# Optimization experiments

Hardware: AMD Instinct MI355X
Metric: run time of the kernel (lower is better)

## Reference

```python
import jax, jax.numpy as jnp
import numpy as np
import math

B, S, D = 2, 2048, 1024
H = 16
DK = D // H  # dim_k == dim_v == 64


def setup_inputs() -> dict:
    key = jax.random.key(0)
    ks = jax.random.split(key, 8)
    scale = 1.0 / math.sqrt(D)
    inp = {
        "query": jax.random.normal(ks[0], (B, S, D), dtype=jnp.float32),
        "key": jax.random.normal(ks[1], (B, S, D), dtype=jnp.float32),
        "value": jax.random.normal(ks[2], (B, S, D), dtype=jnp.float32),
        # stacked per-head projection weights (torch Linear y = x @ W.T; here stored as [H, D, DK])
        "Wq": jax.random.uniform(ks[3], (H, D, DK), dtype=jnp.float32, minval=-scale, maxval=scale),
        "Wk": jax.random.uniform(ks[4], (H, D, DK), dtype=jnp.float32, minval=-scale, maxval=scale),
        "Wv": jax.random.uniform(ks[5], (H, D, DK), dtype=jnp.float32, minval=-scale, maxval=scale),
        "Wo": jax.random.uniform(ks[6], (D, H * DK), dtype=jnp.float32, minval=-scale, maxval=scale),
        "bo": jax.random.uniform(ks[7], (D,), dtype=jnp.float32, minval=-scale, maxval=scale),
    }
    return inp


def reference(query, key, value, Wq, Wk, Wv, Wo, bo):
    # per-head projections, batched over heads via einsum
    q = jnp.einsum("bsd,hdk->bhsk", query, Wq)   # [B,H,S,DK]
    k = jnp.einsum("btd,hdk->bhtk", key, Wk)     # [B,H,S,DK]
    v = jnp.einsum("btd,hdv->bhtv", value, Wv)   # [B,H,S,DK]
    scores = jnp.einsum("bhsk,bhtk->bhst", q, k) / jnp.sqrt(jnp.float32(DK))
    # causal mask (is_causal=True): strictly upper triangle -> -inf
    causal = jnp.tril(jnp.ones((S, S), dtype=bool))  # True = keep
    scores = jnp.where(causal[None, None], scores, -jnp.inf)
    attn = jax.nn.softmax(scores, axis=-1)
    # NaN correction (no-op under pure causal masking, kept for faithfulness)
    attn = jnp.where(jnp.isnan(attn), 0.0, attn)
    out = jnp.einsum("bhst,bhtv->bhsv", attn, v)  # [B,H,S,DK]
    out = jnp.transpose(out, (0, 2, 1, 3)).reshape(B, S, H * DK)  # concat heads
    return out @ Wo.T + bo
```

## Files before the change

### kernel.cpp

```cpp
#include <hip/hip_runtime.h>


#define B_ 2
#define S_ 2048
#define D_ 1024
#define H_ 16
#define DK_ 64
#define NEG_BIG (-1e30f)

typedef unsigned short u16;
typedef __attribute__((ext_vector_type(8))) short bf16x8;
typedef __attribute__((ext_vector_type(4))) float f32x4;

__device__ __forceinline__ float b2f(u16 v) {
    union { unsigned u; float f; } x; x.u = ((unsigned)v) << 16; return x.f;
}
__device__ __forceinline__ u16 f2b(float f) {
    union { float f; unsigned u; } x; x.f = f;
    unsigned r = x.u + 0x7fff + ((x.u >> 16) & 1);
    return (u16)(r >> 16);
}
__device__ __forceinline__ u16 f2b_fast(float f) {
    union { float f; unsigned u; } x; x.f = f;
    return (u16)((x.u + 0x8000u) >> 16);
}

__device__ __forceinline__ bool is_f32(const void* p) {
    const unsigned* u = (const unsigned*)p;
    int cnt = 0;
#pragma unroll
    for (int i = 0; i < 64; i++) {
        unsigned e = (u[i * 8] >> 7) & 0xFFu;
        cnt += (e >= 110u && e <= 134u) ? 1 : 0;
    }
    return cnt < 32;
}

template<bool F32>
__device__ __forceinline__ bf16x8 load8(const void* p, size_t idx) {
    if constexpr (F32) {
        const float* f = (const float*)p + idx;
        float4 a = *(const float4*)f;
        float4 b = *(const float4*)(f + 4);
        bf16x8 r;
        ((u16*)&r)[0] = f2b(a.x); ((u16*)&r)[1] = f2b(a.y);
        ((u16*)&r)[2] = f2b(a.z); ((u16*)&r)[3] = f2b(a.w);
        ((u16*)&r)[4] = f2b(b.x); ((u16*)&r)[5] = f2b(b.y);
        ((u16*)&r)[6] = f2b(b.z); ((u16*)&r)[7] = f2b(b.w);
        return r;
    } else {
        return *(const bf16x8*)((const u16*)p + idx);
    }
}

__global__ __launch_bounds__(256) void wtrans(const void* Wq, const void* Wk, const void* Wv,
                                              u16* WqT, u16* WkT, u16* WvT) {
    __shared__ __align__(16) u16 Ts[64][72];
    const int t = threadIdx.x;
    const int k0 = blockIdx.x * 64;
    const int h = blockIdx.y;
    const int wsel = blockIdx.z;
    const void* W = (wsel == 0) ? Wq : (wsel == 1) ? Wk : Wv;
    u16* WT = (wsel == 0) ? WqT : (wsel == 1) ? WkT : WvT;
    const bool wf = is_f32(W);

    const int drow = t >> 2, c0 = (t & 3) * 16;
    size_t sidx = ((size_t)h * D_ + k0 + drow) * DK_ + c0;
    bf16x8 v0, v1;
    if (wf) { v0 = load8<true >(W, sidx); v1 = load8<true >(W, sidx + 8); }
    else    { v0 = load8<false>(W, sidx); v1 = load8<false>(W, sidx + 8); }
    *(bf16x8*)&Ts[drow][c0]     = v0;
    *(bf16x8*)&Ts[drow][c0 + 8] = v1;
    __syncthreads();

    const int nrow = t >> 2, kc0 = (t & 3) * 16;
    u16 tmp[16];
#pragma unroll
    for (int j = 0; j < 16; j++) tmp[j] = Ts[kc0 + j][nrow];
    u16* dst = &WT[((size_t)h * DK_ + nrow) * D_ + k0 + kc0];
    *(bf16x8*)&dst[0] = *(const bf16x8*)&tmp[0];
    *(bf16x8*)&dst[8] = *(const bf16x8*)&tmp[8];
}

template<bool AF32>
__device__ void qproj_body(const void* A, const u16* WT, u16* Qt, int bb,
                           u16 (*As)[64][72], u16 (*Wt)[64][72]) {
    const int tid = threadIdx.x, mt = blockIdx.x, h = blockIdx.y;
    const int w = tid >> 6, lane = tid & 63, quad = lane >> 4, ln = lane & 15;
    const int s0 = mt * 64;
    const int row = tid >> 3, col = (tid & 7) * 8;
    const int row1 = row + 32;
    const int brow = tid >> 2, bc0 = (tid & 3) * 16;
    const size_t wbase = ((size_t)h * DK_ + brow) * D_ + bc0;

    bf16x8 areg0, areg1, breg0, breg1;
    areg0 = load8<AF32>(A, ((size_t)bb * S_ + s0 + row ) * D_ + col);
    areg1 = load8<AF32>(A, ((size_t)bb * S_ + s0 + row1) * D_ + col);
    breg0 = *(const bf16x8*)&WT[wbase];
    breg1 = *(const bf16x8*)&WT[wbase + 8];

    f32x4 acc[4];
#pragma unroll
    for (int t = 0; t < 4; t++)
#pragma unroll
        for (int r = 0; r < 4; r++) acc[t][r] = 0.f;

    int buf = 0;
    for (int k0 = 0; k0 < D_; k0 += 64, buf ^= 1) {
        *(bf16x8*)&As[buf][row ][col] = areg0;
        *(bf16x8*)&As[buf][row1][col] = areg1;
        *(bf16x8*)&Wt[buf][brow][bc0    ] = breg0;
        *(bf16x8*)&Wt[buf][brow][bc0 + 8] = breg1;
        __syncthreads();
        if (k0 + 64 < D_) {
            areg0 = load8<AF32>(A, ((size_t)bb * S_ + s0 + row ) * D_ + k0 + 64 + col);
            areg1 = load8<AF32>(A, ((size_t)bb * S_ + s0 + row1) * D_ + k0 + 64 + col);
            breg0 = *(const bf16x8*)&WT[wbase + k0 + 64];
            breg1 = *(const bf16x8*)&WT[wbase + k0 + 64 + 8];
        }
#pragma unroll
        for (int kk = 0; kk < 2; kk++) {
            bf16x8 a = *(const bf16x8*)&As[buf][w * 16 + ln][kk * 32 + quad * 8];
#pragma unroll
            for (int t = 0; t < 4; t++) {
                bf16x8 bm = *(const bf16x8*)&Wt[buf][t * 16 + ln][kk * 32 + quad * 8];
                acc[t] = __builtin_amdgcn_mfma_f32_16x16x32_bf16(a, bm, acc[t], 0, 0, 0);
            }
        }
    }

#pragma unroll
    for (int t = 0; t < 4; t++)
#pragma unroll
        for (int r = 0; r < 4; r++)
            Qt[((size_t)bb * S_ + s0 + w * 16 + quad * 4 + r) * D_ + h * DK_ + t * 16 + ln] =
                f2b(acc[t][r] * 0.125f);
}

__global__ __launch_bounds__(256) void qproj(const void* query, const u16* WqT, u16* Qt) {
    __shared__ __align__(16) u16 As[2][64][72];
    __shared__ __align__(16) u16 Wt[2][64][72];
    const int bb = blockIdx.z;
    if (is_f32(query)) qproj_body<true >(query, WqT, Qt, bb, As, Wt);
    else               qproj_body<false>(query, WqT, Qt, bb, As, Wt);
}

template<bool AF32>
__device__ void projkv_body(const void* A, const u16* WT, u16* Ko, u16* VTo,
                            int bb, int which, u16 (*As)[64][72], u16 (*Wt)[64][72]) {
    const int tid = threadIdx.x, mt = blockIdx.x, h = blockIdx.y;
    const int w = tid >> 6, lane = tid & 63, quad = lane >> 4, ln = lane & 15;
    const int s0 = mt * 64;
    const int row = tid >> 3, col = (tid & 7) * 8;
    const int row1 = row + 32;
    const int brow = tid >> 2, bc0 = (tid & 3) * 16;
    const size_t wbase = ((size_t)h * DK_ + brow) * D_ + bc0;

    bf16x8 areg0, areg1, breg0, breg1;
    areg0 = load8<AF32>(A, ((size_t)bb * S_ + s0 + row ) * D_ + col);
    areg1 = load8<AF32>(A, ((size_t)bb * S_ + s0 + row1) * D_ + col);
    breg0 = *(const bf16x8*)&WT[wbase];
    breg1 = *(const bf16x8*)&WT[wbase + 8];

    f32x4 acc[4];
#pragma unroll
    for (int t = 0; t < 4; t++)
#pragma unroll
        for (int r = 0; r < 4; r++) acc[t][r] = 0.f;

    int buf = 0;
    for (int k0 = 0; k0 < D_; k0 += 64, buf ^= 1) {
        *(bf16x8*)&As[buf][row ][col] = areg0;
        *(bf16x8*)&As[buf][row1][col] = areg1;
        *(bf16x8*)&Wt[buf][brow][bc0    ] = breg0;
        *(bf16x8*)&Wt[buf][brow][bc0 + 8] = breg1;
        __syncthreads();
        if (k0 + 64 < D_) {
            areg0 = load8<AF32>(A, ((size_t)bb * S_ + s0 + row ) * D_ + k0 + 64 + col);
            areg1 = load8<AF32>(A, ((size_t)bb * S_ + s0 + row1) * D_ + k0 + 64 + col);
            breg0 = *(const bf16x8*)&WT[wbase + k0 + 64];
            breg1 = *(const bf16x8*)&WT[wbase + k0 + 64 + 8];
        }
#pragma unroll
        for (int kk = 0; kk < 2; kk++) {
            bf16x8 a = *(const bf16x8*)&As[buf][w * 16 + ln][kk * 32 + quad * 8];
#pragma unroll
            for (int t = 0; t < 4; t++) {
                bf16x8 bm = *(const bf16x8*)&Wt[buf][t * 16 + ln][kk * 32 + quad * 8];
                acc[t] = __builtin_amdgcn_mfma_f32_16x16x32_bf16(a, bm, acc[t], 0, 0, 0);
            }
        }
    }

    if (which == 0) {
#pragma unroll
        for (int t = 0; t < 4; t++)
#pragma unroll
            for (int r = 0; r < 4; r++)
                Ko[((size_t)h * S_ + s0 + w * 16 + quad * 4 + r) * DK_ + t * 16 + ln] =
                    f2b(acc[t][r]);
    } else {
#pragma unroll
        for (int t = 0; t < 4; t++)
#pragma unroll
            for (int r = 0; r < 4; r++)
                Wt[0][t * 16 + ln][w * 16 + quad * 4 + r] = f2b(acc[t][r]);
        __syncthreads();
        *(bf16x8*)&VTo[((size_t)h * DK_ + row ) * S_ + s0 + col] = *(const bf16x8*)&Wt[0][row ][col];
        *(bf16x8*)&VTo[((size_t)h * DK_ + row1) * S_ + s0 + col] = *(const bf16x8*)&Wt[0][row1][col];
    }
}

__global__ __launch_bounds__(256) void projkv(const void* key, const void* value,
                                              const u16* WkT, const u16* WvT,
                                              u16* KVbase, int bb) {
    __shared__ __align__(16) u16 As[2][64][72];
    __shared__ __align__(16) u16 Wt[2][64][72];
    const int which = blockIdx.z;
    const void* A = which ? value : key;
    const u16* WT = which ? WvT : WkT;
    u16* Ko  = KVbase;
    u16* VTo = KVbase + (size_t)H_ * S_ * DK_;
    if (is_f32(A)) projkv_body<true >(A, WT, Ko, VTo, bb, which, As, Wt);
    else           projkv_body<false>(A, WT, Ko, VTo, bb, which, As, Wt);
}

__global__ __launch_bounds__(256) void flashq(u16* __restrict__ Xq,
                                              const u16* __restrict__ KV,
                                              int bb0, size_t zstride) {
    __shared__ __align__(16) u16 BufA[2][64][72];
    __shared__ __align__(16) u16 BufB[2][64][72];
    __shared__ __align__(16) u16 Ps[4][32][72];
    const int tid = threadIdx.x;
    const int bx = (int)blockIdx.x;
    const int qt = (blockIdx.z & 1) ? bx : ((int)gridDim.x - 1 - bx);
    const int h = blockIdx.y;
    const int bb = bb0 + blockIdx.z;
    const u16* Kb  = KV + (size_t)blockIdx.z * zstride;
    const u16* VTb = Kb + (size_t)H_ * S_ * DK_;
    const int w = tid >> 6, lane = tid & 63, quad = lane >> 4, ln = lane & 15;
    const int s0 = qt * 128;
    const int row = tid >> 3, col = (tid & 7) * 8;
    const int row1 = row + 32;
    const int j0max = 2 * qt;
    const int jmax  = 2 * qt + 1;

    bf16x8 kreg0 = *(const bf16x8*)&Kb [((size_t)h * S_  + row ) * DK_ + col];
    bf16x8 kreg1 = *(const bf16x8*)&Kb [((size_t)h * S_  + row1) * DK_ + col];
    bf16x8 vreg0 = *(const bf16x8*)&VTb[((size_t)h * DK_ + row ) * S_  + col];
    bf16x8 vreg1 = *(const bf16x8*)&VTb[((size_t)h * DK_ + row1) * S_  + col];

    *(bf16x8*)&BufA[0][row ][col] = *(const bf16x8*)&Xq[((size_t)bb * S_ + s0 + row ) * D_ + h * DK_ + col];
    *(bf16x8*)&BufA[0][row1][col] = *(const bf16x8*)&Xq[((size_t)bb * S_ + s0 + row1) * D_ + h * DK_ + col];
    *(bf16x8*)&BufA[1][row ][col] = *(const bf16x8*)&Xq[((size_t)bb * S_ + s0 + 64 + row ) * D_ + h * DK_ + col];
    *(bf16x8*)&BufA[1][row1][col] = *(const bf16x8*)&Xq[((size_t)bb * S_ + s0 + 64 + row1) * D_ + h * DK_ + col];
    __syncthreads();
    bf16x8 qa0_0 = *(const bf16x8*)&BufA[0][w * 16 + ln][quad * 8];
    bf16x8 qa1_0 = *(const bf16x8*)&BufA[0][w * 16 + ln][32 + quad * 8];
    bf16x8 qa0_1 = *(const bf16x8*)&BufA[1][w * 16 + ln][quad * 8];
    bf16x8 qa1_1 = *(const bf16x8*)&BufA[1][w * 16 + ln][32 + quad * 8];
    __syncthreads();

    f32x4 O0[4], O1[4];
    float psum0[4], psum1[4];
#pragma unroll
    for (int t = 0; t < 4; t++)
#pragma unroll
        for (int r = 0; r < 4; r++) { O0[t][r] = 0.f; O1[t][r] = 0.f; }
#pragma unroll
    for (int r = 0; r < 4; r++) { psum0[r] = 0.f; psum1[r] = 0.f; }

    for (int j = 0; j <= jmax; j++) {
        const int buf = j & 1;
        *(bf16x8*)&BufA[buf][row ][col] = kreg0;
        *(bf16x8*)&BufA[buf][row1][col] = kreg1;
        *(bf16x8*)&BufB[buf][row ][col] = vreg0;
        *(bf16x8*)&BufB[buf][row1][col] = vreg1;
        __syncthreads();

        if (j < jmax) {
            kreg0 = *(const bf16x8*)&Kb [((size_t)h * S_  + (j + 1) * 64 + row ) * DK_ + col];
            kreg1 = *(const bf16x8*)&Kb [((size_t)h * S_  + (j + 1) * 64 + row1) * DK_ + col];
            vreg0 = *(const bf16x8*)&VTb[((size_t)h * DK_ + row ) * S_ + (j + 1) * 64 + col];
            vreg1 = *(const bf16x8*)&VTb[((size_t)h * DK_ + row1) * S_ + (j + 1) * 64 + col];
        }

        const bool act0 = (j <= j0max);

        if (act0) {
            f32x4 sf[4];
#pragma unroll
            for (int t = 0; t < 4; t++)
#pragma unroll
                for (int r = 0; r < 4; r++) sf[t][r] = 0.f;
#pragma unroll
            for (int kk = 0; kk < 2; kk++) {
                bf16x8 a = kk ? qa1_0 : qa0_0;
#pragma unroll
                for (int t = 0; t < 4; t++) {
                    bf16x8 bm = *(const bf16x8*)&BufA[buf][t * 16 + ln][kk * 32 + quad * 8];
                    sf[t] = __builtin_amdgcn_mfma_f32_16x16x32_bf16(a, bm, sf[t], 0, 0, 0);
                }
            }
            if (j == j0max) {
#pragma unroll
                for (int t = 0; t < 4; t++) {
                    int keyl = t * 16 + ln;
#pragma unroll
                    for (int r = 0; r < 4; r++) {
                        int qr = w * 16 + quad * 4 + r;
                        if (keyl > qr) sf[t][r] = NEG_BIG;
                    }
                }
            }
#pragma unroll
            for (int t = 0; t < 4; t++)
#pragma unroll
                for (int r = 0; r < 4; r++) {
                    float p = __expf(sf[t][r]);
                    psum0[r] += p;
                    Ps[w][quad * 4 + r][t * 16 + ln] = f2b_fast(p);
                }
        }

        {
            f32x4 sf[4];
#pragma unroll
            for (int t = 0; t < 4; t++)
#pragma unroll
                for (int r = 0; r < 4; r++) sf[t][r] = 0.f;
#pragma unroll
            for (int kk = 0; kk < 2; kk++) {
                bf16x8 a = kk ? qa1_1 : qa0_1;
#pragma unroll
                for (int t = 0; t < 4; t++) {
                    bf16x8 bm = *(const bf16x8*)&BufA[buf][t * 16 + ln][kk * 32 + quad * 8];
                    sf[t] = __builtin_amdgcn_mfma_f32_16x16x32_bf16(a, bm, sf[t], 0, 0, 0);
                }
            }
            if (j == jmax) {
#pragma unroll
                for (int t = 0; t < 4; t++) {
                    int keyl = t * 16 + ln;
#pragma unroll
                    for (int r = 0; r < 4; r++) {
                        int qr = w * 16 + quad * 4 + r;
                        if (keyl > qr) sf[t][r] = NEG_BIG;
                    }
                }
            }
#pragma unroll
            for (int t = 0; t < 4; t++)
#pragma unroll
                for (int r = 0; r < 4; r++) {
                    float p = __expf(sf[t][r]);
                    psum1[r] += p;
                    Ps[w][16 + quad * 4 + r][t * 16 + ln] = f2b_fast(p);
                }
        }
        __syncthreads();

        if (act0) {
#pragma unroll
            for (int kk = 0; kk < 2; kk++) {
                bf16x8 a = *(const bf16x8*)&Ps[w][ln][kk * 32 + quad * 8];
#pragma unroll
                for (int t = 0; t < 4; t++) {
                    bf16x8 bm = *(const bf16x8*)&BufB[buf][t * 16 + ln][kk * 32 + quad * 8];
                    O0[t] = __builtin_amdgcn_mfma_f32_16x16x32_bf16(a, bm, O0[t], 0, 0, 0);
                }
            }
        }
#pragma unroll
        for (int kk = 0; kk < 2; kk++) {
            bf16x8 a = *(const bf16x8*)&Ps[w][16 + ln][kk * 32 + quad * 8];
#pragma unroll
            for (int t = 0; t < 4; t++) {
                bf16x8 bm = *(const bf16x8*)&BufB[buf][t * 16 + ln][kk * 32 + quad * 8];
                O1[t] = __builtin_amdgcn_mfma_f32_16x16x32_bf16(a, bm, O1[t], 0, 0, 0);
            }
        }
    }

#pragma unroll
    for (int r = 0; r < 4; r++) {
        float s = psum0[r];
        s += __shfl_xor(s, 1, 64);
        s += __shfl_xor(s, 2, 64);
        s += __shfl_xor(s, 4, 64);
        s += __shfl_xor(s, 8, 64);
        float inv = 1.0f / s;
        int sr = s0 + w * 16 + quad * 4 + r;
#pragma unroll
        for (int t = 0; t < 4; t++) {
            Xq[((size_t)bb * S_ + sr) * D_ + h * DK_ + t * 16 + ln] = f2b(O0[t][r] * inv);
        }
    }
#pragma unroll
    for (int r = 0; r < 4; r++) {
        float s = psum1[r];
        s += __shfl_xor(s, 1, 64);
        s += __shfl_xor(s, 2, 64);
        s += __shfl_xor(s, 4, 64);
        s += __shfl_xor(s, 8, 64);
        float inv = 1.0f / s;
        int sr = s0 + 64 + w * 16 + quad * 4 + r;
#pragma unroll
        for (int t = 0; t < 4; t++) {
            Xq[((size_t)bb * S_ + sr) * D_ + h * DK_ + t * 16 + ln] = f2b(O1[t][r] * inv);
        }
    }
}

__global__ __launch_bounds__(256) void copyx(const u16* __restrict__ src,
                                             u16* __restrict__ dst) {
    size_t i = ((size_t)blockIdx.x * 256 + threadIdx.x) * 8;
    *(bf16x8*)&dst[i] = *(const bf16x8*)&src[i];
}

template<bool WF32>
__device__ void outgemm_body(const u16* X, const void* Wo, const void* bo, bool bf32,
                             float* Y, u16 (*As)[64][72], u16 (*Bs)[64][72]) {
    const int tid = threadIdx.x, mt = blockIdx.x, nt = blockIdx.y;
    const int w = tid >> 6, lane = tid & 63, quad = lane >> 4, ln = lane & 15;
    const int m0 = mt * 64, n0 = nt * 64;
    const int row = tid >> 3, col = (tid & 7) * 8;
    const int row1 = row + 32;

    bf16x8 areg0, areg1, wreg0, wreg1;
    areg0 = *(const bf16x8*)&X[(size_t)(m0 + row ) * D_ + col];
    areg1 = *(const bf16x8*)&X[(size_t)(m0 + row1) * D_ + col];
    wreg0 = load8<WF32>(Wo, (size_t)(n0 + row ) * D_ + col);
    wreg1 = load8<WF32>(Wo, (size_t)(n0 + row1) * D_ + col);

    f32x4 acc[4];
#pragma unroll
    for (int t = 0; t < 4; t++)
#pragma unroll
        for (int r = 0; r < 4; r++) acc[t][r] = 0.f;

    int buf = 0;
    for (int k0 = 0; k0 < D_; k0 += 64, buf ^= 1) {
        *(bf16x8*)&As[buf][row ][col] = areg0;
        *(bf16x8*)&As[buf][row1][col] = areg1;
        *(bf16x8*)&Bs[buf][row ][col] = wreg0;
        *(bf16x8*)&Bs[buf][row1][col] = wreg1;
        __syncthreads();
        if (k0 + 64 < D_) {
            areg0 = *(const bf16x8*)&X[(size_t)(m0 + row ) * D_ + k0 + 64 + col];
            areg1 = *(const bf16x8*)&X[(size_t)(m0 + row1) * D_ + k0 + 64 + col];
            wreg0 = load8<WF32>(Wo, (size_t)(n0 + row ) * D_ + k0 + 64 + col);
            wreg1 = load8<WF32>(Wo, (size_t)(n0 + row1) * D_ + k0 + 64 + col);
        }
#pragma unroll
        for (int kk = 0; kk < 2; kk++) {
            bf16x8 a = *(const bf16x8*)&As[buf][w * 16 + ln][kk * 32 + quad * 8];
#pragma unroll
            for (int t = 0; t < 4; t++) {
                bf16x8 bm = *(const bf16x8*)&Bs[buf][t * 16 + ln][kk * 32 + quad * 8];
                acc[t] = __builtin_amdgcn_mfma_f32_16x16x32_bf16(a, bm, acc[t], 0, 0, 0);
            }
        }
    }

#pragma unroll
    for (int t = 0; t < 4; t++) {
        int n = n0 + t * 16 + ln;
        float bias = bf32 ? ((const float*)bo)[n] : b2f(((const u16*)bo)[n]);
#pragma unroll
        for (int r = 0; r < 4; r++) {
            int m = m0 + w * 16 + quad * 4 + r;
            Y[(size_t)m * D_ + n] = acc[t][r] + bias;
        }
    }
}

__global__ __launch_bounds__(256) void outgemm(const u16* __restrict__ X,
                                               const void* Wo, const void* bo,
                                               float* __restrict__ Y) {
    __shared__ __align__(16) u16 As[2][64][72];
    __shared__ __align__(16) u16 Bs[2][64][72];
    const bool wf = is_f32(Wo), bf = is_f32(bo);
    if (wf) outgemm_body<true >(X, Wo, bo, bf, Y, As, Bs);
    else    outgemm_body<false>(X, Wo, bo, bf, Y, As, Bs);
}

extern "C" void kernel_launch(void* const* d_in, const int* in_sizes, int n_in,
                              void* d_out, int out_size, void* d_ws, size_t ws_size,
                              hipStream_t stream) {
    const void* q  = d_in[0];
    const void* k  = d_in[1];
    const void* v  = d_in[2];
    const void* Wq = d_in[3];
    const void* Wk = d_in[4];
    const void* Wv = d_in[5];
    const void* Wo = d_in[6];
    const void* bo = d_in[7];

    u16* ob   = (u16*)d_out;
    u16* Xq   = ob;
    u16* WkT  = ob + (size_t)4 * 1024 * 1024;
    u16* WvT  = WkT + (size_t)1024 * 1024;
    u16* WqT  = WvT + (size_t)1024 * 1024;
    u16* ws16 = (u16*)d_ws;
    const size_t kvblk = (size_t)2 * H_ * S_ * DK_;
    const bool bigws = ws_size >= (size_t)16 * 1024 * 1024;

    wtrans<<<dim3(D_ / 64, H_, 3), dim3(256), 0, stream>>>(Wq, Wk, Wv, WqT, WkT, WvT);
    qproj<<<dim3(S_ / 64, H_, B_), dim3(256), 0, stream>>>(q, WqT, Xq);
    if (bigws) {
        projkv<<<dim3(S_ / 64, H_, 2), dim3(256), 0, stream>>>(k, v, WkT, WvT, ws16, 0);
        projkv<<<dim3(S_ / 64, H_, 2), dim3(256), 0, stream>>>(k, v, WkT, WvT, ws16 + kvblk, 1);
        flashq<<<dim3(S_ / 128, H_, 2), dim3(256), 0, stream>>>(Xq, ws16, 0, kvblk);
    } else {
        projkv<<<dim3(S_ / 64, H_, 2), dim3(256), 0, stream>>>(k, v, WkT, WvT, ws16, 0);
        flashq<<<dim3(S_ / 128, H_, 1), dim3(256), 0, stream>>>(Xq, ws16, 0, 0);
        projkv<<<dim3(S_ / 64, H_, 2), dim3(256), 0, stream>>>(k, v, WkT, WvT, ws16, 1);
        flashq<<<dim3(S_ / 128, H_, 1), dim3(256), 0, stream>>>(Xq, ws16, 1, 0);
    }
    copyx<<<dim3((B_ * S_ * D_) / (256 * 8)), dim3(256), 0, stream>>>(Xq, ws16);
    outgemm<<<dim3((B_ * S_) / 64, D_ / 64), dim3(256), 0, stream>>>(ws16, Wo, bo, (float*)d_out);
}
```

Baseline: 284.1 us.

## Split flash attention query tile across 8 waves with 512-thread blocks

The flash attention kernel now launches 512 threads per block. Each wave owns 16 query rows of one 64-row half, where before each of 4 waves processed two 16-row halves in sequence. Per-thread K/V staging drops to one vector load each and per-wave accumulators are halved, which cuts register pressure and doubles wave-level parallelism for latency hiding. In exchange, the waves for the first half sit idle on the final K/V tile, and synchronisation now spans more waves.

```diff
diff --git a/kernel.cpp b/kernel.cpp
--- a/kernel.cpp
+++ b/kernel.cpp
@@ -225,12 +225,12 @@
     else           projkv_body<false>(A, WT, Ko, VTo, bb, which, As, Wt);
 }
 
-__global__ __launch_bounds__(256) void flashq(u16* __restrict__ Xq,
+__global__ __launch_bounds__(512) void flashq(u16* __restrict__ Xq,
                                               const u16* __restrict__ KV,
                                               int bb0, size_t zstride) {
     __shared__ __align__(16) u16 BufA[2][64][72];
     __shared__ __align__(16) u16 BufB[2][64][72];
-    __shared__ __align__(16) u16 Ps[4][32][72];
+    __shared__ __align__(16) u16 Ps[8][16][72];
     const int tid = threadIdx.x;
     const int bx = (int)blockIdx.x;
     const int qt = (blockIdx.z & 1) ? bx : ((int)gridDim.x - 1 - bx);
@@ -239,55 +239,46 @@
     const u16* Kb  = KV + (size_t)blockIdx.z * zstride;
     const u16* VTb = Kb + (size_t)H_ * S_ * DK_;
     const int w = tid >> 6, lane = tid & 63, quad = lane >> 4, ln = lane & 15;
+    const int half = w >> 2, wr = w & 3;
     const int s0 = qt * 128;
-    const int row = tid >> 3, col = (tid & 7) * 8;
-    const int row1 = row + 32;
+    const int srow = tid >> 3, scol = (tid & 7) * 8;
     const int j0max = 2 * qt;
     const int jmax  = 2 * qt + 1;
-
-    bf16x8 kreg0 = *(const bf16x8*)&Kb [((size_t)h * S_  + row ) * DK_ + col];
-    bf16x8 kreg1 = *(const bf16x8*)&Kb [((size_t)h * S_  + row1) * DK_ + col];
-    bf16x8 vreg0 = *(const bf16x8*)&VTb[((size_t)h * DK_ + row ) * S_  + col];
-    bf16x8 vreg1 = *(const bf16x8*)&VTb[((size_t)h * DK_ + row1) * S_  + col];
-
-    *(bf16x8*)&BufA[0][row ][col] = *(const bf16x8*)&Xq[((size_t)bb * S_ + s0 + row ) * D_ + h * DK_ + col];
-    *(bf16x8*)&BufA[0][row1][col] = *(const bf16x8*)&Xq[((size_t)bb * S_ + s0 + row1) * D_ + h * DK_ + col];
-    *(bf16x8*)&BufA[1][row ][col] = *(const bf16x8*)&Xq[((size_t)bb * S_ + s0 + 64 + row ) * D_ + h * DK_ + col];
-    *(bf16x8*)&BufA[1][row1][col] = *(const bf16x8*)&Xq[((size_t)bb * S_ + s0 + 64 + row1) * D_ + h * DK_ + col];
+    const int jdiag = half ? jmax : j0max;
+
+    bf16x8 kreg = *(const bf16x8*)&Kb [((size_t)h * S_  + srow) * DK_ + scol];
+    bf16x8 vreg = *(const bf16x8*)&VTb[((size_t)h * DK_ + srow) * S_  + scol];
+
+    *(bf16x8*)&BufA[0][srow][scol] = *(const bf16x8*)&Xq[((size_t)bb * S_ + s0 + srow) * D_ + h * DK_ + scol];
+    *(bf16x8*)&BufA[1][srow][scol] = *(const bf16x8*)&Xq[((size_t)bb * S_ + s0 + 64 + srow) * D_ + h * DK_ + scol];
     __syncthreads();
-    bf16x8 qa0_0 = *(const bf16x8*)&BufA[0][w * 16 + ln][quad * 8];
-    bf16x8 qa1_0 = *(const bf16x8*)&BufA[0][w * 16 + ln][32 + quad * 8];
-    bf16x8 qa0_1 = *(const bf16x8*)&BufA[1][w * 16 + ln][quad * 8];
-    bf16x8 qa1_1 = *(const bf16x8*)&BufA[1][w * 16 + ln][32 + quad * 8];
+    bf16x8 qa0 = *(const bf16x8*)&BufA[half][wr * 16 + ln][quad * 8];
+    bf16x8 qa1 = *(const bf16x8*)&BufA[half][wr * 16 + ln][32 + quad * 8];
     __syncthreads();
 
-    f32x4 O0[4], O1[4];
-    float psum0[4], psum1[4];
+    f32x4 O[4];
+    float psum[4];
 #pragma unroll
     for (int t = 0; t < 4; t++)
 #pragma unroll
-        for (int r = 0; r < 4; r++) { O0[t][r] = 0.f; O1[t][r] = 0.f; }
-#pragma unroll
-    for (int r = 0; r < 4; r++) { psum0[r] = 0.f; psum1[r] = 0.f; }
+        for (int r = 0; r < 4; r++) O[t][r] = 0.f;
+#pragma unroll
+    for (int r = 0; r < 4; r++) psum[r] = 0.f;
 
     for (int j = 0; j <= jmax; j++) {
         const int buf = j & 1;
-        *(bf16x8*)&BufA[buf][row ][col] = kreg0;
-        *(bf16x8*)&BufA[buf][row1][col] = kreg1;
-        *(bf16x8*)&BufB[buf][row ][col] = vreg0;
-        *(bf16x8*)&BufB[buf][row1][col] = vreg1;
+        *(bf16x8*)&BufA[buf][srow][scol] = kreg;
+        *(bf16x8*)&BufB[buf][srow][scol] = vreg;
         __syncthreads();
 
         if (j < jmax) {
-            kreg0 = *(const bf16x8*)&Kb [((size_t)h * S_  + (j + 1) * 64 + row ) * DK_ + col];
-            kreg1 = *(const bf16x8*)&Kb [((size_t)h * S_  + (j + 1) * 64 + row1) * DK_ + col];
-            vreg0 = *(const bf16x8*)&VTb[((size_t)h * DK_ + row ) * S_ + (j + 1) * 64 + col];
-            vreg1 = *(const bf16x8*)&VTb[((size_t)h * DK_ + row1) * S_ + (j + 1) * 64 + col];
-        }
-
-        const bool act0 = (j <= j0max);
-
-        if (act0) {
+            kreg = *(const bf16x8*)&Kb [((size_t)h * S_  + (j + 1) * 64 + srow) * DK_ + scol];
+            vreg = *(const bf16x8*)&VTb[((size_t)h * DK_ + srow) * S_ + (j + 1) * 64 + scol];
+        }
+
+        const bool act = half ? true : (j <= j0max);
+
+        if (act) {
             f32x4 sf[4];
 #pragma unroll
             for (int t = 0; t < 4; t++)
@@ -295,20 +286,20 @@
                 for (int r = 0; r < 4; r++) sf[t][r] = 0.f;
 #pragma unroll
             for (int kk = 0; kk < 2; kk++) {
-                bf16x8 a = kk ? qa1_0 : qa0_0;
+                bf16x8 a = kk ? qa1 : qa0;
 #pragma unroll
                 for (int t = 0; t < 4; t++) {
                     bf16x8 bm = *(const bf16x8*)&BufA[buf][t * 16 + ln][kk * 32 + quad * 8];
                     sf[t] = __builtin_amdgcn_mfma_f32_16x16x32_bf16(a, bm, sf[t], 0, 0, 0);
                 }
             }
-            if (j == j0max) {
+            if (j == jdiag) {
 #pragma unroll
                 for (int t = 0; t < 4; t++) {
                     int keyl = t * 16 + ln;
 #pragma unroll
                     for (int r = 0; r < 4; r++) {
-                        int qr = w * 16 + quad * 4 + r;
+                        int qr = wr * 16 + quad * 4 + r;
                         if (keyl > qr) sf[t][r] = NEG_BIG;
                     }
                 }
@@ -318,96 +309,37 @@
 #pragma unroll
                 for (int r = 0; r < 4; r++) {
                     float p = __expf(sf[t][r]);
-                    psum0[r] += p;
+                    psum[r] += p;
                     Ps[w][quad * 4 + r][t * 16 + ln] = f2b_fast(p);
                 }
         }
-
-        {
-            f32x4 sf[4];
-#pragma unroll
-            for (int t = 0; t < 4; t++)
-#pragma unroll
-                for (int r = 0; r < 4; r++) sf[t][r] = 0.f;
-#pragma unroll
-            for (int kk = 0; kk < 2; kk++) {
-                bf16x8 a = kk ? qa1_1 : qa0_1;
-#pragma unroll
-                for (int t = 0; t < 4; t++) {
-                    bf16x8 bm = *(const bf16x8*)&BufA[buf][t * 16 + ln][kk * 32 + quad * 8];
-                    sf[t] = __builtin_amdgcn_mfma_f32_16x16x32_bf16(a, bm, sf[t], 0, 0, 0);
-                }
-            }
-            if (j == jmax) {
-#pragma unroll
-                for (int t = 0; t < 4; t++) {
-                    int keyl = t * 16 + ln;
-#pragma unroll
-                    for (int r = 0; r < 4; r++) {
-                        int qr = w * 16 + quad * 4 + r;
-                        if (keyl > qr) sf[t][r] = NEG_BIG;
-                    }
-                }
-            }
-#pragma unroll
-            for (int t = 0; t < 4; t++)
-#pragma unroll
-                for (int r = 0; r < 4; r++) {
-                    float p = __expf(sf[t][r]);
-                    psum1[r] += p;
-                    Ps[w][16 + quad * 4 + r][t * 16 + ln] = f2b_fast(p);
-                }
-        }
-        __syncthreads();
-
-        if (act0) {
+        __syncthreads();
+
+        if (act) {
 #pragma unroll
             for (int kk = 0; kk < 2; kk++) {
                 bf16x8 a = *(const bf16x8*)&Ps[w][ln][kk * 32 + quad * 8];
 #pragma unroll
                 for (int t = 0; t < 4; t++) {
                     bf16x8 bm = *(const bf16x8*)&BufB[buf][t * 16 + ln][kk * 32 + quad * 8];
-                    O0[t] = __builtin_amdgcn_mfma_f32_16x16x32_bf16(a, bm, O0[t], 0, 0, 0);
+                    O[t] = __builtin_amdgcn_mfma_f32_16x16x32_bf16(a, bm, O[t], 0, 0, 0);
                 }
             }
         }
-#pragma unroll
-        for (int kk = 0; kk < 2; kk++) {
-            bf16x8 a = *(const bf16x8*)&Ps[w][16 + ln][kk * 32 + quad * 8];
-#pragma unroll
-            for (int t = 0; t < 4; t++) {
-                bf16x8 bm = *(const bf16x8*)&BufB[buf][t * 16 + ln][kk * 32 + quad * 8];
-                O1[t] = __builtin_amdgcn_mfma_f32_16x16x32_bf16(a, bm, O1[t], 0, 0, 0);
-            }
-        }
     }
 
 #pragma unroll
     for (int r = 0; r < 4; r++) {
-        float s = psum0[r];
+        float s = psum[r];
         s += __shfl_xor(s, 1, 64);
         s += __shfl_xor(s, 2, 64);
         s += __shfl_xor(s, 4, 64);
         s += __shfl_xor(s, 8, 64);
         float inv = 1.0f / s;
-        int sr = s0 + w * 16 + quad * 4 + r;
+        int sr = s0 + half * 64 + wr * 16 + quad * 4 + r;
 #pragma unroll
         for (int t = 0; t < 4; t++) {
-            Xq[((size_t)bb * S_ + sr) * D_ + h * DK_ + t * 16 + ln] = f2b(O0[t][r] * inv);
-        }
-    }
-#pragma unroll
-    for (int r = 0; r < 4; r++) {
-        float s = psum1[r];
-        s += __shfl_xor(s, 1, 64);
-        s += __shfl_xor(s, 2, 64);
-        s += __shfl_xor(s, 4, 64);
-        s += __shfl_xor(s, 8, 64);
-        float inv = 1.0f / s;
-        int sr = s0 + 64 + w * 16 + quad * 4 + r;
-#pragma unroll
-        for (int t = 0; t < 4; t++) {
-            Xq[((size_t)bb * S_ + sr) * D_ + h * DK_ + t * 16 + ln] = f2b(O1[t][r] * inv);
+            Xq[((size_t)bb * S_ + sr) * D_ + h * DK_ + t * 16 + ln] = f2b(O[t][r] * inv);
         }
     }
 }
@@ -511,12 +443,12 @@
     if (bigws) {
         projkv<<<dim3(S_ / 64, H_, 2), dim3(256), 0, stream>>>(k, v, WkT, WvT, ws16, 0);
         projkv<<<dim3(S_ / 64, H_, 2), dim3(256), 0, stream>>>(k, v, WkT, WvT, ws16 + kvblk, 1);
-        flashq<<<dim3(S_ / 128, H_, 2), dim3(256), 0, stream>>>(Xq, ws16, 0, kvblk);
+        flashq<<<dim3(S_ / 128, H_, 2), dim3(512), 0, stream>>>(Xq, ws16, 0, kvblk);
     } else {
         projkv<<<dim3(S_ / 64, H_, 2), dim3(256), 0, stream>>>(k, v, WkT, WvT, ws16, 0);
-        flashq<<<dim3(S_ / 128, H_, 1), dim3(256), 0, stream>>>(Xq, ws16, 0, 0);
+        flashq<<<dim3(S_ / 128, H_, 1), dim3(512), 0, stream>>>(Xq, ws16, 0, 0);
         projkv<<<dim3(S_ / 64, H_, 2), dim3(256), 0, stream>>>(k, v, WkT, WvT, ws16, 1);
-        flashq<<<dim3(S_ / 128, H_, 1), dim3(256), 0, stream>>>(Xq, ws16, 1, 0);
+        flashq<<<dim3(S_ / 128, H_, 1), dim3(512), 0, stream>>>(Xq, ws16, 1, 0);
     }
     copyx<<<dim3((B_ * S_ * D_) / (256 * 8)), dim3(256), 0, stream>>>(Xq, ws16);
     outgemm<<<dim3((B_ * S_) / 64, D_ / 64), dim3(256), 0, stream>>>(ws16, Wo, bo, (float*)d_out);
```

New measurement: 271.9 us. 4.3% less time.
